# Optimization experiments

Hardware: AMD Instinct MI355X
Metric: run time of the kernel (lower is better)

## Reference

```python
import jax, jax.numpy as jnp
import numpy as np

B = 32          # batch of input networks (INRs)
D = 128         # d_hid
H = 8           # attention heads
DH = D // H
L = 3           # RT layers
DOUT = 10
LAYOUT = [2, 32, 32, 1]          # INR layer layout -> graph nodes
N = 2 + 32 + 32 + 1              # 67 nodes
POS_LAYOUT = [1, 1, 32, 32, 1]   # [1]*layout[0] + layout[1:-1] + [1]*layout[-1]


def _ln(x, g, b, eps=1e-5):
    m = x.mean(-1, keepdims=True)
    v = ((x - m) ** 2).mean(-1, keepdims=True)
    return (x - m) * jax.lax.rsqrt(v + eps) * g + b


def _gelu(x):
    return jax.nn.gelu(x, approximate=False)


def setup_inputs() -> dict:
    key = jax.random.key(0)
    cnt = [0]
    def nk():
        cnt[0] += 1
        return jax.random.fold_in(key, cnt[0])
    def rn(shape, s=0.02):
        return (s * jax.random.normal(nk(), shape)).astype(jnp.float32)
    z = lambda *s: jnp.zeros(s, jnp.float32)
    o = lambda *s: jnp.ones(s, jnp.float32)
    inp = dict(
        w0=rn((B, 2, 32, 1), 1.0), w1=rn((B, 32, 32, 1), 1.0), w2=rn((B, 32, 1, 1), 1.0),
        b0=rn((B, 32, 1), 1.0), b1=rn((B, 32, 1), 1.0), b2=rn((B, 1, 1), 1.0),
        pw_W=rn((1, D)), pw_b=z(D), pb_W=rn((1, D)), pb_b=z(D),
        node_in_W=rn((D, D)), node_in_b=z(D), edge_in_W=rn((D, D)), edge_in_b=z(D),
        pos_embed=rn((len(POS_LAYOUT), D), 1.0),
        aln_g=o(L, D), aln_b=z(L, D),
        Wqkv_n=rn((L, D, 3 * D)), Wqkv_e=rn((L, D, 3 * D)), Wao=rn((L, D, D)), bao=z(L, D),
        Wl0=rn((L, D, D)), bl0=z(L, D),
        nln_g=o(L, D), nln_b=z(L, D),
        nW1=rn((L, D, 2 * D)), nb1=z(L, 2 * D), nW2=rn((L, 2 * D, D)), nb2=z(L, D),
        eln_g=o(L, D), eln_b=z(L, D),
        We=rn((L, 2 * D, D)), be=z(L, D),
        Ws=rn((L, D, D)), bs=z(L, D), Wt=rn((L, D, D)), bt=z(L, D),
        Wer=rn((L, D, D)), Wec=rn((L, D, D)), We1=rn((L, D, D)), be1=z(L, D),
        Wel0=rn((L, D, D)), bel0=z(L, D),
        mln_g=o(L, D), mln_b=z(L, D),
        mW1=rn((L, D, 2 * D)), mb1=z(L, 2 * D), mW2=rn((L, 2 * D, D)), mb2=z(L, D),
        Wo1=rn((D, D)), bo1=z(D), Wo2=rn((D, DOUT)), bo2=z(DOUT),
    )
    return inp


def _forward(w0, w1, w2, b0, b1, b2, pw_W, pw_b, pb_W, pb_b, node_in_W, node_in_b,
             edge_in_W, edge_in_b, pos_embed, aln_g, aln_b, Wqkv_n, Wqkv_e, Wao, bao,
             Wl0, bl0, nln_g, nln_b, nW1, nb1, nW2, nb2, eln_g, eln_b, We, be, Ws, bs,
             Wt, bt, Wer, Wec, We1, be1, Wel0, bel0, mln_g, mln_b, mW1, mb1, mW2, mb2,
             Wo1, bo1, Wo2, bo2):
    # ---- GraphConstructor / batch_to_graphs (layout [2,32,32,1], offsets 0/2/34/66) ----
    nf = jnp.zeros((B, N, 1), w0.dtype)
    ef = jnp.zeros((B, N, N, 1), w0.dtype)
    ef = ef.at[:, 0:2, 2:34].set(w0).at[:, 2:34, 34:66].set(w1).at[:, 34:66, 66:67].set(w2)
    nf = nf.at[:, 2:34].set(b0).at[:, 34:66].set(b1).at[:, 66:67].set(b2)
    node = nf @ pb_W + pb_b            # proj_bias: Linear(1, D)
    edge = ef @ pw_W + pw_b            # proj_weight: Linear(1, D)
    node = node @ node_in_W + node_in_b
    edge = edge @ edge_in_W + edge_in_b
    pos = jnp.concatenate([jnp.broadcast_to(pos_embed[i], (n, D))
                           for i, n in enumerate(POS_LAYOUT)], axis=0)  # [N, D]
    node = node + pos

    scale = 1.0 / np.sqrt(DH)
    for l in range(L):
        # ---- RTAttention (edge-biased multi-head attention) ----
        h = _ln(node, aln_g[l], aln_b[l])
        qkv_n = (h @ Wqkv_n[l]).reshape(B, N, H, 3, DH).transpose(0, 2, 3, 1, 4)       # b H 3 n dh
        qn, kn, vn = qkv_n[:, :, 0], qkv_n[:, :, 1], qkv_n[:, :, 2]
        qkv_e = (edge @ Wqkv_e[l]).reshape(B, N, N, H, 3, DH).transpose(0, 3, 4, 1, 2, 5)  # b H 3 n m dh
        q = qn[:, :, :, None, :] + qkv_e[:, :, 0]
        k = kn[:, :, None, :, :] + qkv_e[:, :, 1]
        v = vn[:, :, None, :, :] + qkv_e[:, :, 2]
        att = jax.nn.softmax((q * k).sum(-1) * scale, axis=-1)                          # b H n m
        o = jnp.einsum('bhnm,bhnmd->bhnd', att, v).transpose(0, 2, 1, 3).reshape(B, N, D)
        node = node + ((o @ Wao[l] + bao[l]) @ Wl0[l] + bl0[l])
        node = node + (_gelu(_ln(node, nln_g[l], nln_b[l]) @ nW1[l] + nb1[l]) @ nW2[l] + nb2[l])
        # ---- Edge update (EdgeMLP with forward/reversed edges + node/row/col terms) ----
        en = _ln(edge, eln_g[l], eln_b[l])
        m = jnp.concatenate([en, en.transpose(0, 2, 1, 3)], axis=-1) @ We[l] + be[l]
        m = m + (node @ Ws[l] + bs[l])[:, :, None, :] + (node @ Wt[l] + bt[l])[:, None, :, :]
        m = m + en.mean(2, keepdims=True) @ Wer[l] + en.mean(1, keepdims=True) @ Wec[l]
        m = _gelu(m) @ We1[l] + be1[l]
        edge = edge + (m @ Wel0[l] + bel0[l])
        edge = edge + (_gelu(_ln(edge, mln_g[l], mln_b[l]) @ mW1[l] + mb1[l]) @ mW2[l] + mb2[l])

    g = node.mean(1)                                        # mean pooling over nodes
    return jax.nn.relu(g @ Wo1 + bo1) @ Wo2 + bo2           # [B, DOUT]


def reference(w0, w1, w2, b0, b1, b2, pw_W, pw_b, pb_W, pb_b, node_in_W, node_in_b,
              edge_in_W, edge_in_b, pos_embed, aln_g, aln_b, Wqkv_n, Wqkv_e, Wao, bao,
              Wl0, bl0, nln_g, nln_b, nW1, nb1, nW2, nb2, eln_g, eln_b, We, be, Ws, bs,
              Wt, bt, Wer, Wec, We1, be1, Wel0, bel0, mln_g, mln_b, mW1, mb1, mW2, mb2,
              Wo1, bo1, Wo2, bo2):
    return _forward(w0, w1, w2, b0, b1, b2, pw_W, pw_b, pb_W, pb_b, node_in_W, node_in_b,
                    edge_in_W, edge_in_b, pos_embed, aln_g, aln_b, Wqkv_n, Wqkv_e, Wao, bao,
                    Wl0, bl0, nln_g, nln_b, nW1, nb1, nW2, nb2, eln_g, eln_b, We, be, Ws, bs,
                    Wt, bt, Wer, Wec, We1, be1, Wel0, bel0, mln_g, mln_b, mW1, mb1, mW2, mb2,
                    Wo1, bo1, Wo2, bo2)
```

## Files before the change

### kernel.cpp

```cpp
#include <hip/hip_runtime.h>
#include <math.h>

constexpr int B_ = 32, N_ = 67, D_ = 128, H_ = 8, DH_ = 16, L_ = 3;
constexpr int NN_ = N_ * N_;
constexpr int RN_ = B_ * N_;
constexpr int RE_ = B_ * NN_;
constexpr int DOUT_ = 10;

typedef __attribute__((ext_vector_type(8))) short short8;
typedef __attribute__((ext_vector_type(4))) float f32x4;

__device__ __forceinline__ float gelu_f(float x) {
  float u = x * (0.7978845608028654f + 0.035677408136f * x * x);
  float e = __expf(-2.f * u);
  return x * (1.f / (1.f + e));
}
__device__ __forceinline__ ushort f2b(float x) {
  union { float f; unsigned u; } v; v.f = x;
  return (ushort)((v.u + 0x7FFFu + ((v.u >> 16) & 1u)) >> 16);
}
__device__ __forceinline__ float b2f(ushort u) {
  union { unsigned u; float f; } v; v.u = (unsigned)u << 16; return v.f;
}

__global__ void k_comb(const float* __restrict__ Wao, const float* __restrict__ bao,
                       const float* __restrict__ Wl0, const float* __restrict__ bl0,
                       const float* __restrict__ We1, const float* __restrict__ be1,
                       const float* __restrict__ Wel0, const float* __restrict__ bel0,
                       float* WcN, float* bcN, float* WcE, float* bcE) {
  int t = blockIdx.x * blockDim.x + threadIdx.x;
  const int half = L_ * D_ * D_;
  if (t >= 2 * half) return;
  int which = t / half;
  int u = t - which * half;
  int l = u / (D_ * D_);
  int ij = u - l * (D_ * D_);
  int i = ij >> 7, j = ij & 127;
  const float* A  = (which == 0 ? Wao : We1) + (size_t)l * D_ * D_;
  const float* Bm = (which == 0 ? Wl0 : Wel0) + (size_t)l * D_ * D_;
  float s = 0.f;
  for (int k = 0; k < D_; k++) s += A[i * D_ + k] * Bm[k * D_ + j];
  if (which == 0) WcN[u] = s; else WcE[u] = s;
  if (i == 0) {
    const float* ba = (which == 0 ? bao : be1) + l * D_;
    const float* bl = (which == 0 ? bl0 : bel0) + l * D_;
    float sb = 0.f;
    for (int k = 0; k < D_; k++) sb += ba[k] * Bm[k * D_ + j];
    if (which == 0) bcN[l * D_ + j] = sb + bl[j]; else bcE[l * D_ + j] = sb + bl[j];
  }
}

__device__ __forceinline__ float enc_src(const float* src, int K, int C, int NKS, int r, int l) {
  int frag = r >> 9;
  int within = r & 511;
  int lane = within >> 3, j = within & 7;
  int cf = frag / NKS, ks = frag - cf * NKS;
  int k = ks * 32 + (lane >> 4) * 8 + j;
  int c = cf * 16 + (lane & 15);
  return src[(size_t)l * K * C + (size_t)k * C + c];
}

__global__ void k_prepw(const float* __restrict__ Wqkve, const float* __restrict__ We,
                        const float* __restrict__ WcE, const float* __restrict__ mW1,
                        const float* __restrict__ mW2,
                        ushort* wq, ushort* we, ushort* wce, ushort* w1, ushort* w2) {
  int t = blockIdx.x * 256 + threadIdx.x;
  const int S0 = L_ * 49152, S1 = L_ * 32768, S2 = L_ * 16384, S3 = L_ * 32768, S4 = L_ * 32768;
  if (t < S0) { int l = t / 49152, r = t % 49152; wq[t]  = f2b(enc_src(Wqkve, 128, 384, 4, r, l)); return; }
  t -= S0;
  if (t < S1) { int l = t / 32768, r = t % 32768; we[t]  = f2b(enc_src(We,   256, 128, 8, r, l)); return; }
  t -= S1;
  if (t < S2) { int l = t / 16384, r = t % 16384; wce[t] = f2b(enc_src(WcE,  128, 128, 4, r, l)); return; }
  t -= S2;
  if (t < S3) { int l = t / 32768, r = t % 32768; w1[t]  = f2b(enc_src(mW1,  128, 256, 4, r, l)); return; }
  t -= S3;
  if (t < S4) { int l = t / 32768, r = t % 32768; w2[t]  = f2b(enc_src(mW2,  256, 128, 8, r, l)); return; }
}

__global__ void k_vecs(const float* pbW, const float* pbb, const float* niW, const float* nib,
                       const float* pwW, const float* pwb, const float* eiW, const float* eib,
                       float* vecs) {
  int j = threadIdx.x;
  if (j >= D_) return;
  float u = 0, c = 0, v = 0, ce = 0;
  for (int k = 0; k < D_; k++) {
    u  += pbW[k] * niW[k * D_ + j];
    c  += pbb[k] * niW[k * D_ + j];
    v  += pwW[k] * eiW[k * D_ + j];
    ce += pwb[k] * eiW[k * D_ + j];
  }
  vecs[j] = u; vecs[D_ + j] = c + nib[j]; vecs[2 * D_ + j] = v; vecs[3 * D_ + j] = ce + eib[j];
}

__global__ void k_init_node(const float* __restrict__ b0, const float* __restrict__ b1,
                            const float* __restrict__ b2, const float* __restrict__ vecs,
                            const float* __restrict__ pos, float* __restrict__ node) {
  int idx = blockIdx.x * blockDim.x + threadIdx.x;
  if (idx >= RN_ * D_) return;
  int r = idx >> 7, d = idx & 127;
  int b = r / N_, n = r - b * N_;
  float nf = 0.f;
  if (n >= 2 && n < 34)       nf = b0[b * 32 + n - 2];
  else if (n >= 34 && n < 66) nf = b1[b * 32 + n - 34];
  else if (n == 66)           nf = b2[b];
  int pr = (n == 0) ? 0 : (n == 1) ? 1 : (n < 34) ? 2 : (n < 66) ? 3 : 4;
  node[idx] = nf * vecs[d] + vecs[D_ + d] + pos[pr * D_ + d];
}

__global__ void k_init_edge(const float* __restrict__ w0, const float* __restrict__ w1,
                            const float* __restrict__ w2, const float* __restrict__ vecs,
                            ushort* __restrict__ edge) {
  int idx = blockIdx.x * blockDim.x + threadIdx.x;
  if (idx >= RE_ * D_) return;
  int r = idx >> 7, d = idx & 127;
  int b = r / NN_;
  int rem = r - b * NN_;
  int n = rem / N_, m = rem - n * N_;
  float ef = 0.f;
  if (n < 2)        { if (m >= 2 && m < 34)  ef = w0[(b * 2 + n) * 32 + (m - 2)]; }
  else if (n < 34)  { if (m >= 34 && m < 66) ef = w1[(b * 32 + (n - 2)) * 32 + (m - 34)]; }
  else if (n < 66)  { if (m == 66)           ef = w2[b * 32 + (n - 34)]; }
  edge[idx] = f2b(ef * vecs[2 * D_ + d] + vecs[3 * D_ + d]);
}

__global__ __launch_bounds__(256) void k_lnqkv(
    const float* __restrict__ node, const float* __restrict__ g, const float* __restrict__ bb,
    const float* __restrict__ W, float* __restrict__ out) {
  __shared__ float As[16][68];
  __shared__ float Wsh[16][68];
  __shared__ float stmu[64], strs[64];
  int r0 = blockIdx.x * 64, c0 = blockIdx.y * 64;
  int tid = threadIdx.x;
  {
    int row = tid >> 2, part = tid & 3;
    int gr = r0 + row;
    int grc = (gr < RN_) ? gr : 0;
    const float* x = node + (size_t)grc * 128 + part * 32;
    float s = 0.f, q = 0.f;
#pragma unroll
    for (int i = 0; i < 8; i++) {
      float4 v = *reinterpret_cast<const float4*>(&x[i * 4]);
      s += v.x + v.y + v.z + v.w;
      q += v.x * v.x + v.y * v.y + v.z * v.z + v.w * v.w;
    }
    for (int o = 1; o < 4; o <<= 1) { s += __shfl_xor(s, o); q += __shfl_xor(q, o); }
    if (part == 0) {
      float mu = s * (1.f / 128.f);
      stmu[row] = mu;
      strs[row] = rsqrtf(q * (1.f / 128.f) - mu * mu + 1e-5f);
    }
  }
  __syncthreads();
  int tr = tid >> 4, tc = tid & 15;
  float acc[4][4] = {};
  for (int kk = 0; kk < 128; kk += 16) {
#pragma unroll
    for (int i = 0; i < 4; i++) {
      int lin = tid + i * 256;
      int r_in = lin >> 4, k_in = lin & 15;
      int r = r0 + r_in;
      float v = 0.f;
      if (r < RN_) {
        int k = kk + k_in;
        v = (node[(size_t)r * 128 + k] - stmu[r_in]) * strs[r_in] * g[k] + bb[k];
      }
      As[k_in][r_in] = v;
    }
#pragma unroll
    for (int i = 0; i < 4; i++) {
      int lin = tid + i * 256;
      int k_in = lin >> 6, c_in = lin & 63;
      Wsh[k_in][c_in] = W[(size_t)(kk + k_in) * 384 + c0 + c_in];
    }
    __syncthreads();
#pragma unroll
    for (int k = 0; k < 16; k++) {
      float4 a4 = *reinterpret_cast<const float4*>(&As[k][tr * 4]);
      float4 b4 = *reinterpret_cast<const float4*>(&Wsh[k][tc * 4]);
      float av[4] = {a4.x, a4.y, a4.z, a4.w};
      float bv[4] = {b4.x, b4.y, b4.z, b4.w};
#pragma unroll
      for (int i = 0; i < 4; i++)
#pragma unroll
        for (int j = 0; j < 4; j++) acc[i][j] += av[i] * bv[j];
    }
    __syncthreads();
  }
#pragma unroll
  for (int i = 0; i < 4; i++) {
    int r = r0 + tr * 4 + i;
    if (r >= RN_) continue;
#pragma unroll
    for (int j = 0; j < 4; j++) {
      int c = c0 + tc * 4 + j;
      out[(size_t)r * 384 + c] = acc[i][j];
    }
  }
}

__global__ __launch_bounds__(256) void k_nodemlp(
    float* __restrict__ node, const float* __restrict__ obuf,
    const float* __restrict__ WcN, const float* __restrict__ bcN,
    const float* __restrict__ g, const float* __restrict__ bb,
    const float* __restrict__ nW1, const float* __restrict__ nb1,
    const float* __restrict__ nW2, const float* __restrict__ nb2) {
  __shared__ float As[16][17];
  __shared__ float Wsh[16][132];
  __shared__ ushort Hs[16][136];
  __shared__ ushort Ts[16][264];
  int r0 = blockIdx.x * 16;
  int tid = threadIdx.x;
  int tr = tid >> 4, tc = tid & 15;
  size_t grow = (size_t)(r0 + tr) * 128;

  auto stageW = [&](const float* src, int ld, int kk, int cbase) {
    int k = tid & 15, cp = tid >> 4;
    const float* s = &src[(size_t)(kk + k) * ld + cbase + cp * 8];
    float* d = &Wsh[k][cp * 8];
#pragma unroll
    for (int j = 0; j < 8; j++) d[j] = s[j];
  };

  float acc[8] = {};
  for (int kk = 0; kk < 128; kk += 16) {
    As[tr][tc] = obuf[grow + kk + tc];
    stageW(WcN, 128, kk, 0);
    __syncthreads();
#pragma unroll
    for (int k = 0; k < 16; k++) {
      float a = As[tr][k];
#pragma unroll
      for (int j = 0; j < 8; j++) acc[j] += a * Wsh[k][tc * 8 + j];
    }
    __syncthreads();
  }
  float nd[8];
  float s = 0.f, q = 0.f;
#pragma unroll
  for (int j = 0; j < 8; j++) {
    int c = tc * 8 + j;
    float v = node[grow + c] + acc[j] + bcN[c];
    nd[j] = v; s += v; q += v * v;
  }
  for (int o = 1; o < 16; o <<= 1) { s += __shfl_xor(s, o); q += __shfl_xor(q, o); }
  float mu = s * (1.f / 128.f);
  float rs = rsqrtf(q * (1.f / 128.f) - mu * mu + 1e-5f);
#pragma unroll
  for (int j = 0; j < 8; j++) {
    int c = tc * 8 + j;
    Hs[tr][c] = f2b((nd[j] - mu) * rs * g[c] + bb[c]);
  }
  for (int ch = 0; ch < 2; ch++) {
    float a2[8] = {};
    for (int kk = 0; kk < 128; kk += 16) {
      __syncthreads();
      stageW(nW1, 256, kk, ch * 128);
      __syncthreads();
#pragma unroll
      for (int k = 0; k < 16; k++) {
        float a = b2f(Hs[tr][kk + k]);
#pragma unroll
        for (int j = 0; j < 8; j++) a2[j] += a * Wsh[k][tc * 8 + j];
      }
    }
#pragma unroll
    for (int j = 0; j < 8; j++) {
      int c = ch * 128 + tc * 8 + j;
      Ts[tr][c] = f2b(gelu_f(a2[j] + nb1[c]));
    }
  }
  float a3[8] = {};
  for (int kk = 0; kk < 256; kk += 16) {
    __syncthreads();
    stageW(nW2, 128, kk, 0);
    __syncthreads();
#pragma unroll
    for (int k = 0; k < 16; k++) {
      float a = b2f(Ts[tr][kk + k]);
#pragma unroll
      for (int j = 0; j < 8; j++) a3[j] += a * Wsh[k][tc * 8 + j];
    }
  }
#pragma unroll
  for (int j = 0; j < 8; j++) {
    int c = tc * 8 + j;
    node[grow + c] = nd[j] + a3[j] + nb2[c];
  }
}

__global__ __launch_bounds__(256) void k_nvec(
    const float* __restrict__ node, const float* __restrict__ rmean, const float* __restrict__ cmean,
    const float* __restrict__ Ws, const float* __restrict__ Wer,
    const float* __restrict__ Wt, const float* __restrict__ Wec,
    const float* __restrict__ bs, const float* __restrict__ be, const float* __restrict__ bt,
    float* __restrict__ rvec, float* __restrict__ cvec) {
  __shared__ float Ash[16][68];
  __shared__ float Wsh[16][68];
  int which = blockIdx.z;
  const float* A2 = which ? cmean : rmean;
  const float* W1 = which ? Wt : Ws;
  const float* W2 = which ? Wec : Wer;
  float* out = which ? cvec : rvec;
  int r0 = blockIdx.x * 64, c0 = blockIdx.y * 64;
  int tid = threadIdx.x, tr = tid >> 4, tc = tid & 15;
  float acc[4][4] = {};
  for (int kk = 0; kk < 256; kk += 16) {
#pragma unroll
    for (int i = 0; i < 4; i++) {
      int lin = tid + i * 256;
      int r_in = lin >> 4, k_in = lin & 15;
      int r = r0 + r_in, k = kk + k_in;
      float v = 0.f;
      if (r < RN_) v = (k < 128) ? node[(size_t)r * 128 + k] : A2[(size_t)r * 128 + (k - 128)];
      Ash[k_in][r_in] = v;
    }
#pragma unroll
    for (int i = 0; i < 4; i++) {
      int lin = tid + i * 256;
      int k_in = lin >> 6, c_in = lin & 63;
      int k = kk + k_in, c = c0 + c_in;
      Wsh[k_in][c_in] = (k < 128) ? W1[(size_t)k * 128 + c] : W2[(size_t)(k - 128) * 128 + c];
    }
    __syncthreads();
#pragma unroll
    for (int k = 0; k < 16; k++) {
      float4 a4 = *reinterpret_cast<const float4*>(&Ash[k][tr * 4]);
      float4 b4 = *reinterpret_cast<const float4*>(&Wsh[k][tc * 4]);
      float av[4] = {a4.x, a4.y, a4.z, a4.w};
      float bv[4] = {b4.x, b4.y, b4.z, b4.w};
#pragma unroll
      for (int i = 0; i < 4; i++)
#pragma unroll
        for (int j = 0; j < 4; j++) acc[i][j] += av[i] * bv[j];
    }
    __syncthreads();
  }
#pragma unroll
  for (int i = 0; i < 4; i++) {
    int r = r0 + tr * 4 + i;
    if (r >= RN_) continue;
#pragma unroll
    for (int j = 0; j < 4; j++) {
      int c = c0 + tc * 4 + j;
      float bias = which ? bt[c] : (bs[c] + be[c]);
      out[(size_t)r * 128 + c] = acc[i][j] + bias;
    }
  }
}

__global__ __launch_bounds__(256, 3) void k_eattn(
    const ushort* __restrict__ edge, const float* __restrict__ qkvn,
    const ushort* __restrict__ wqf,
    const float* __restrict__ gE, const float* __restrict__ bE,
    float* __restrict__ stats, float* __restrict__ rmean,
    float* __restrict__ obuf) {
  __shared__ __align__(16) ushort ed[68 * 128];
  __shared__ __align__(16) ushort Eb[68 * 202];
  __shared__ float qn_s[384];
  __shared__ float sc[4][68];
  __shared__ float red[4][16][4];
  __shared__ float stmu[68], strs[68];
  int bn = blockIdx.x;
  int b = bn / N_;
  int tid = threadIdx.x;
  int w = tid >> 6, lane = tid & 63, lr = lane & 15, lk8 = (lane >> 4) * 8;
  int swz = (lr & 7) << 3;
  int rb = (lane >> 4) * 4;
  size_t ebase = (size_t)bn * N_ * 128;

  for (int i = 0; i < 5; i++) {
    int u = tid + i * 256;
    if (u < 67 * 16) {
      int row = u >> 4, k8 = (u & 15) * 8;
      short8 t = __builtin_nontemporal_load(
          reinterpret_cast<const short8*>(&edge[ebase + (size_t)row * 128 + k8]));
      *reinterpret_cast<short8*>(&ed[row * 128 + (k8 ^ ((row & 7) << 3))]) = t;
      float s = 0.f, q = 0.f;
#pragma unroll
      for (int j = 0; j < 8; j++) { float v = b2f((ushort)t[j]); s += v; q += v * v; }
      for (int o = 8; o; o >>= 1) { s += __shfl_xor(s, o); q += __shfl_xor(q, o); }
      if ((u & 15) == 0) {
        float mu = s * (1.f / 128.f);
        float rs = rsqrtf(q * (1.f / 128.f) - mu * mu + 1e-5f);
        stmu[row] = mu; strs[row] = rs;
        stats[2 * (size_t)(bn * N_ + row)] = mu;
        stats[2 * (size_t)(bn * N_ + row) + 1] = rs;
      }
    }
  }
  for (int i = tid; i < 384; i += 256) qn_s[i] = qkvn[(size_t)bn * 384 + i];
  __syncthreads();
  if (tid < 128) {
    float s = 0.f;
    for (int m = 0; m < 67; m++)
      s += (b2f(ed[m * 128 + (tid ^ ((m & 7) << 3))]) - stmu[m]) * strs[m];
    rmean[(size_t)bn * 128 + tid] = gE[tid] * (s * (1.f / 67.f)) + bE[tid];
  }

  for (int ch = 0; ch < 2; ch++) {
    int h0 = ch * 4;
    f32x4 acc[5][3] = {};
    __builtin_amdgcn_s_setprio(1);
#pragma unroll
    for (int ks = 0; ks < 4; ks++) {
      int kof = ks * 32 + lk8;
      short8 af[5];
#pragma unroll
      for (int rf = 0; rf < 5; rf++)
        af[rf] = *reinterpret_cast<const short8*>(&ed[(rf * 16 + lr) * 128 + (kof ^ swz)]);
#pragma unroll
      for (int cl = 0; cl < 3; cl++) {
        short8 bf = *reinterpret_cast<const short8*>(
            &wqf[(size_t)(((ch * 12 + w * 3 + cl) * 4 + ks) * 64 + lane) * 8]);
#pragma unroll
        for (int rf = 0; rf < 5; rf++)
          acc[rf][cl] = __builtin_amdgcn_mfma_f32_16x16x32_bf16(af[rf], bf, acc[rf][cl], 0, 0, 0);
      }
    }
    __builtin_amdgcn_s_setprio(0);
#pragma unroll
    for (int rf = 0; rf < 5; rf++)
#pragma unroll
      for (int cl = 0; cl < 3; cl++) {
        int colc = (w * 3 + cl) * 16 + lr;
#pragma unroll
        for (int rg = 0; rg < 4; rg++) {
          int er = rf * 16 + rb + rg;
          if (er < 67) Eb[er * 202 + colc] = f2b(acc[rf][cl][rg]);
        }
      }
    __syncthreads();
    for (int idx = tid; idx < 268; idx += 256) {
      int h2 = idx / 67, m = idx - h2 * 67;
      const ushort* e = &Eb[m * 202 + h2 * 48];
      const float* kn = &qkvn[(size_t)(b * N_ + m) * 384 + (h0 + h2) * 48 + 16];
      const float* qn = &qn_s[(h0 + h2) * 48];
      float s2 = 0.f;
#pragma unroll
      for (int d = 0; d < 16; d++)
        s2 += (qn[d] + b2f(e[d])) * (kn[d] + b2f(e[16 + d]));
      sc[h2][m] = s2 * 0.25f;
    }
    __syncthreads();
    {
      float v0 = (lane < 67) ? sc[w][lane] : -1e30f;
      float v1 = (lane < 3) ? sc[w][lane + 64] : -1e30f;
      float mx = fmaxf(v0, v1);
      for (int o = 32; o; o >>= 1) mx = fmaxf(mx, __shfl_xor(mx, o));
      float e0 = (lane < 67) ? __expf(v0 - mx) : 0.f;
      float e1 = (lane < 3) ? __expf(v1 - mx) : 0.f;
      float ss = e0 + e1;
      for (int o = 32; o; o >>= 1) ss += __shfl_xor(ss, o);
      float inv = 1.f / ss;
      if (lane < 67) sc[w][lane] = e0 * inv;
      if (lane < 3) sc[w][lane + 64] = e1 * inv;
    }
    __syncthreads();
    {
      int item = tid >> 2, c = tid & 3;
      int h2 = item >> 4, d = item & 15;
      float p = 0.f;
      for (int m = c; m < 67; m += 4) {
        float v = qkvn[(size_t)(b * N_ + m) * 384 + (h0 + h2) * 48 + 32 + d]
                + b2f(Eb[m * 202 + h2 * 48 + 32 + d]);
        p += sc[h2][m] * v;
      }
      red[h2][d][c] = p;
    }
    __syncthreads();
    if (tid < 64) {
      int h2 = tid >> 4, d = tid & 15;
      obuf[(size_t)bn * 128 + (h0 + h2) * 16 + d] =
          red[h2][d][0] + red[h2][d][1] + red[h2][d][2] + red[h2][d][3];
    }
    __syncthreads();
  }
}

__global__ void k_colmean(const ushort* __restrict__ edge, const float* __restrict__ stats,
                          const float* __restrict__ g, const float* __restrict__ bb,
                          float* __restrict__ cmean) {
  int bm = blockIdx.x;
  int b = bm / N_, m = bm - b * N_;
  int d = threadIdx.x;
  float s = 0.f;
  for (int n = 0; n < N_; n++) {
    size_t r = (size_t)b * NN_ + (size_t)n * N_ + m;
    s += (b2f(edge[r * D_ + d]) - stats[2 * r]) * stats[2 * r + 1];
  }
  cmean[(size_t)bm * D_ + d] = g[d] * (s * (1.f / 67.f)) + bb[d];
}

__global__ __launch_bounds__(256, 2) void k_fedge(
    const ushort* __restrict__ ein, ushort* __restrict__ eout,
    const float* __restrict__ stats,
    const float* __restrict__ gE, const float* __restrict__ bE,
    const ushort* __restrict__ wef,
    const float* __restrict__ rvec, const float* __restrict__ cvec,
    const ushort* __restrict__ wcef,
    const float* __restrict__ bcE,
    const float* __restrict__ gM, const float* __restrict__ bM,
    const ushort* __restrict__ w1f,
    const float* __restrict__ mb1,
    const ushort* __restrict__ w2f,
    const float* __restrict__ mb2) {
  __shared__ __align__(16) ushort As[64 * 256];
  __shared__ __align__(16) ushort mt[64 * 128];
  __shared__ __align__(16) ushort Wb[32 * 512];
  int tid = threadIdx.x;
  int r0 = blockIdx.x * 64;
  int w = tid >> 6, lane = tid & 63, lr = lane & 15, lk8 = (lane >> 4) * 8;
  int swz = (lr & 7) << 3;
  int rb = (lane >> 4) * 4;
  int arow = w * 16 + lr;

  auto stageW = [&](const ushort* src) {
#pragma unroll
    for (int i = 0; i < 8; i++) {
      int u = tid + i * 256;
      short8 t = *reinterpret_cast<const short8*>(&src[(size_t)u * 8]);
      *reinterpret_cast<short8*>(&Wb[u * 8]) = t;
    }
  };

#pragma unroll
  for (int i = 0; i < 8; i++) {
    int u = tid + i * 256;
    int row = u >> 5, c8 = (u & 31) * 8;
    int gr = r0 + row;
    int grc = (gr < RE_) ? gr : 0;
    int cc = c8 & 127;
    short8 t;
    float mu, rs;
    if (c8 < 128) {
      size_t srow = (size_t)grc;
      mu = stats[2 * srow]; rs = stats[2 * srow + 1];
      t = *reinterpret_cast<const short8*>(&ein[srow * 128 + cc]);
    } else {
      int b = grc / NN_; int rem = grc - b * NN_;
      int n = rem / N_, m = rem - n * N_;
      size_t srow = (size_t)b * NN_ + (size_t)m * N_ + n;
      mu = stats[2 * srow]; rs = stats[2 * srow + 1];
      t = __builtin_nontemporal_load(reinterpret_cast<const short8*>(&ein[srow * 128 + cc]));
    }
    short8 r8;
#pragma unroll
    for (int j = 0; j < 8; j++) {
      float v = (b2f((ushort)t[j]) - mu) * rs * gE[cc + j] + bE[cc + j];
      r8[j] = (short)f2b(v);
    }
    *reinterpret_cast<short8*>(&As[row * 256 + (c8 ^ ((row & 7) << 3))]) = r8;
  }
  int rvb[4], cvb[4], grows[4]; bool vr[4];
#pragma unroll
  for (int rg = 0; rg < 4; rg++) {
    int gr = r0 + w * 16 + rb + rg;
    vr[rg] = gr < RE_;
    int grc = vr[rg] ? gr : 0;
    grows[rg] = grc;
    int b = grc / NN_; int rem = grc - b * NN_;
    int n = rem / N_, m = rem - n * N_;
    rvb[rg] = (b * N_ + n) * 128;
    cvb[rg] = (b * N_ + m) * 128;
  }
  __syncthreads();

  for (int h = 0; h < 2; h++) {
    if (h) __syncthreads();
    stageW(wef + (size_t)h * 32 * 512);
    __syncthreads();
    f32x4 acc[4] = {};
    __builtin_amdgcn_s_setprio(1);
#pragma unroll
    for (int ks = 0; ks < 8; ks++) {
      int kof = ks * 32 + lk8;
      short8 af = *reinterpret_cast<const short8*>(&As[arow * 256 + (kof ^ swz)]);
#pragma unroll
      for (int cf = 0; cf < 4; cf++) {
        short8 bf = *reinterpret_cast<const short8*>(&Wb[(cf * 8 + ks) * 512 + lane * 8]);
        acc[cf] = __builtin_amdgcn_mfma_f32_16x16x32_bf16(af, bf, acc[cf], 0, 0, 0);
      }
    }
    __builtin_amdgcn_s_setprio(0);
#pragma unroll
    for (int cf = 0; cf < 4; cf++) {
      int c = (h * 4 + cf) * 16 + lr;
#pragma unroll
      for (int rg = 0; rg < 4; rg++) {
        float v = acc[cf][rg] + rvec[rvb[rg] + c] + cvec[cvb[rg] + c];
        int mrow = w * 16 + rb + rg;
        mt[mrow * 128 + (c ^ ((mrow & 7) << 3))] = f2b(gelu_f(v));
      }
    }
  }

  __syncthreads();
  stageW(wcef);
  __syncthreads();
  f32x4 e1[8] = {};
  __builtin_amdgcn_s_setprio(1);
#pragma unroll
  for (int ks = 0; ks < 4; ks++) {
    int kof = ks * 32 + lk8;
    short8 af = *reinterpret_cast<const short8*>(&mt[arow * 128 + (kof ^ swz)]);
#pragma unroll
    for (int cf = 0; cf < 8; cf++) {
      short8 bf = *reinterpret_cast<const short8*>(&Wb[(cf * 4 + ks) * 512 + lane * 8]);
      e1[cf] = __builtin_amdgcn_mfma_f32_16x16x32_bf16(af, bf, e1[cf], 0, 0, 0);
    }
  }
  __builtin_amdgcn_s_setprio(0);
  {
    float sr[4] = {0, 0, 0, 0}, qr[4] = {0, 0, 0, 0};
#pragma unroll
    for (int cf = 0; cf < 8; cf++) {
      int c = cf * 16 + lr;
#pragma unroll
      for (int rg = 0; rg < 4; rg++) {
        float v = e1[cf][rg] + bcE[c] + b2f(ein[(size_t)grows[rg] * 128 + c]);
        e1[cf][rg] = v;
        sr[rg] += v; qr[rg] += v * v;
      }
    }
#pragma unroll
    for (int rg = 0; rg < 4; rg++) {
      float s = sr[rg], q = qr[rg];
      for (int o = 8; o; o >>= 1) { s += __shfl_xor(s, o); q += __shfl_xor(q, o); }
      float mu = s * (1.f / 128.f);
      float rs = rsqrtf(q * (1.f / 128.f) - mu * mu + 1e-5f);
#pragma unroll
      for (int cf = 0; cf < 8; cf++) {
        int c = cf * 16 + lr;
        int mrow = w * 16 + rb + rg;
        mt[mrow * 128 + (c ^ ((mrow & 7) << 3))] =
            f2b((e1[cf][rg] - mu) * rs * gM[c] + bM[c]);
      }
    }
  }

  for (int h = 0; h < 2; h++) {
    __syncthreads();
    stageW(w1f + (size_t)h * 32 * 512);
    __syncthreads();
    f32x4 acc[8] = {};
    __builtin_amdgcn_s_setprio(1);
#pragma unroll
    for (int ks = 0; ks < 4; ks++) {
      int kof = ks * 32 + lk8;
      short8 af = *reinterpret_cast<const short8*>(&mt[arow * 128 + (kof ^ swz)]);
#pragma unroll
      for (int cf = 0; cf < 8; cf++) {
        short8 bf = *reinterpret_cast<const short8*>(&Wb[(cf * 4 + ks) * 512 + lane * 8]);
        acc[cf] = __builtin_amdgcn_mfma_f32_16x16x32_bf16(af, bf, acc[cf], 0, 0, 0);
      }
    }
    __builtin_amdgcn_s_setprio(0);
#pragma unroll
    for (int cf = 0; cf < 8; cf++) {
      int c2 = (h * 8 + cf) * 16 + lr;
#pragma unroll
      for (int rg = 0; rg < 4; rg++) {
        int mrow = w * 16 + rb + rg;
        As[mrow * 256 + (c2 ^ ((mrow & 7) << 3))] = f2b(gelu_f(acc[cf][rg] + mb1[c2]));
      }
    }
  }

  for (int h = 0; h < 2; h++) {
    __syncthreads();
    stageW(w2f + (size_t)h * 32 * 512);
    __syncthreads();
    f32x4 acc[4] = {};
    __builtin_amdgcn_s_setprio(1);
#pragma unroll
    for (int ks = 0; ks < 8; ks++) {
      int kof = ks * 32 + lk8;
      short8 af = *reinterpret_cast<const short8*>(&As[arow * 256 + (kof ^ swz)]);
#pragma unroll
      for (int cf = 0; cf < 4; cf++) {
        short8 bf = *reinterpret_cast<const short8*>(&Wb[(cf * 8 + ks) * 512 + lane * 8]);
        acc[cf] = __builtin_amdgcn_mfma_f32_16x16x32_bf16(af, bf, acc[cf], 0, 0, 0);
      }
    }
    __builtin_amdgcn_s_setprio(0);
#pragma unroll
    for (int cf = 0; cf < 4; cf++) {
      int cg = h * 4 + cf;
      int c = cg * 16 + lr;
#pragma unroll
      for (int rg = 0; rg < 4; rg++) {
        int mrow = w * 16 + rb + rg;
        mt[mrow * 128 + (c ^ ((mrow & 7) << 3))] = f2b(e1[cg][rg] + acc[cf][rg] + mb2[c]);
      }
    }
  }

  __syncthreads();
#pragma unroll
  for (int p = 0; p < 4; p++) {
    int u = p * 256 + tid;
    int row = u >> 4, col8 = (u & 15) * 8;
    int gr = r0 + row;
    if (gr < RE_) {
      short8 v = *reinterpret_cast<const short8*>(&mt[row * 128 + (col8 ^ ((row & 7) << 3))]);
      __builtin_nontemporal_store(v, reinterpret_cast<short8*>(&eout[(size_t)gr * 128 + col8]));
    }
  }
}

__global__ void k_head(const float* __restrict__ node, const float* __restrict__ Wo1,
                       const float* __restrict__ bo1, const float* __restrict__ Wo2,
                       const float* __restrict__ bo2, float* __restrict__ out) {
  int b = blockIdx.x;
  int tid = threadIdx.x;
  __shared__ float gsh[D_];
  __shared__ float h1[D_];
  float s = 0.f;
  for (int n = 0; n < N_; n++) s += node[((size_t)b * N_ + n) * D_ + tid];
  gsh[tid] = s * (1.f / 67.f);
  __syncthreads();
  float a = 0.f;
  for (int k = 0; k < D_; k++) a += gsh[k] * Wo1[k * D_ + tid];
  h1[tid] = fmaxf(a + bo1[tid], 0.f);
  __syncthreads();
  if (tid < DOUT_) {
    float r = 0.f;
    for (int k = 0; k < D_; k++) r += h1[k] * Wo2[k * DOUT_ + tid];
    out[b * DOUT_ + tid] = r + bo2[tid];
  }
}

extern "C" void kernel_launch(void* const* d_in, const int* in_sizes, int n_in,
                              void* d_out, int out_size, void* d_ws, size_t ws_size,
                              hipStream_t stream) {
  const float* w0   = (const float*)d_in[0];
  const float* w1   = (const float*)d_in[1];
  const float* w2   = (const float*)d_in[2];
  const float* b0   = (const float*)d_in[3];
  const float* b1   = (const float*)d_in[4];
  const float* b2   = (const float*)d_in[5];
  const float* pwW  = (const float*)d_in[6];
  const float* pwb  = (const float*)d_in[7];
  const float* pbW  = (const float*)d_in[8];
  const float* pbb  = (const float*)d_in[9];
  const float* niW  = (const float*)d_in[10];
  const float* nib  = (const float*)d_in[11];
  const float* eiW  = (const float*)d_in[12];
  const float* eib  = (const float*)d_in[13];
  const float* pos  = (const float*)d_in[14];
  const float* alng = (const float*)d_in[15];
  const float* alnb = (const float*)d_in[16];
  const float* Wqkvn= (const float*)d_in[17];
  const float* Wqkve= (const float*)d_in[18];
  const float* Wao  = (const float*)d_in[19];
  const float* bao  = (const float*)d_in[20];
  const float* Wl0  = (const float*)d_in[21];
  const float* bl0  = (const float*)d_in[22];
  const float* nlng = (const float*)d_in[23];
  const float* nlnb = (const float*)d_in[24];
  const float* nW1  = (const float*)d_in[25];
  const float* nb1  = (const float*)d_in[26];
  const float* nW2  = (const float*)d_in[27];
  const float* nb2  = (const float*)d_in[28];
  const float* elng = (const float*)d_in[29];
  const float* elnb = (const float*)d_in[30];
  const float* We   = (const float*)d_in[31];
  const float* be   = (const float*)d_in[32];
  const float* Ws   = (const float*)d_in[33];
  const float* bs   = (const float*)d_in[34];
  const float* Wt   = (const float*)d_in[35];
  const float* bt   = (const float*)d_in[36];
  const float* Wer  = (const float*)d_in[37];
  const float* Wec  = (const float*)d_in[38];
  const float* We1  = (const float*)d_in[39];
  const float* be1  = (const float*)d_in[40];
  const float* Wel0 = (const float*)d_in[41];
  const float* bel0 = (const float*)d_in[42];
  const float* mlng = (const float*)d_in[43];
  const float* mlnb = (const float*)d_in[44];
  const float* mW1  = (const float*)d_in[45];
  const float* mb1  = (const float*)d_in[46];
  const float* mW2  = (const float*)d_in[47];
  const float* mb2  = (const float*)d_in[48];
  const float* Wo1  = (const float*)d_in[49];
  const float* bo1  = (const float*)d_in[50];
  const float* Wo2  = (const float*)d_in[51];
  const float* bo2  = (const float*)d_in[52];
  float* outp = (float*)d_out;

  const size_t E = (size_t)RE_ * D_;
  const size_t NODE = (size_t)RN_ * D_;
  const int DD = D_ * D_;

  float* ws = (float*)d_ws;
  size_t off = 0;
  auto alloc = [&](size_t nf) { float* p = ws + off; off += nf; return p; };
  ushort* edgeA = (ushort*)alloc(E / 2);
  ushort* edgeB = (ushort*)alloc(E / 2);
  float* stats = alloc(2 * (size_t)RE_);
  float* node  = alloc(NODE);
  float* qkvn  = alloc(3 * NODE);
  float* obuf  = alloc(NODE);
  float* rmean = alloc(NODE);
  float* cmean = alloc(NODE);
  float* rvec  = alloc(NODE);
  float* cvec  = alloc(NODE);
  float* WcN   = alloc((size_t)L_ * DD);
  float* bcN   = alloc((size_t)L_ * D_);
  float* WcE   = alloc((size_t)L_ * DD);
  float* bcE   = alloc((size_t)L_ * D_);
  float* vecs  = alloc(4 * D_);
  ushort* wbf   = (ushort*)alloc(245760);
  ushort* wq_fm = wbf;
  ushort* we_fm = wq_fm + (size_t)L_ * 49152;
  ushort* wce_fm= we_fm + (size_t)L_ * 32768;
  ushort* w1_fm = wce_fm + (size_t)L_ * 16384;
  ushort* w2_fm = w1_fm + (size_t)L_ * 32768;
  (void)ws_size; (void)in_sizes; (void)n_in; (void)out_size;

  k_comb<<<(2 * L_ * DD + 255) / 256, 256, 0, stream>>>(Wao, bao, Wl0, bl0, We1, be1, Wel0, bel0,
                                                        WcN, bcN, WcE, bcE);
  k_prepw<<<1920, 256, 0, stream>>>(Wqkve, We, WcE, mW1, mW2, wq_fm, we_fm, wce_fm, w1_fm, w2_fm);
  k_vecs<<<1, 128, 0, stream>>>(pbW, pbb, niW, nib, pwW, pwb, eiW, eib, vecs);
  k_init_node<<<(RN_ * D_ + 255) / 256, 256, 0, stream>>>(b0, b1, b2, vecs, pos, node);
  k_init_edge<<<(int)((E + 255) / 256), 256, 0, stream>>>(w0, w1, w2, vecs, edgeA);

  const int GE = (RE_ + 63) / 64;
  const int GN = (RN_ + 63) / 64;
  const int GM = RN_ / 16;

  for (int l = 0; l < L_; l++) {
    ushort* ein  = (l & 1) ? edgeB : edgeA;
    ushort* eout = (l & 1) ? edgeA : edgeB;
    const float* Wqn = Wqkvn + (size_t)l * D_ * 384;

    k_lnqkv<<<dim3(GN, 6), 256, 0, stream>>>(node, alng + l * D_, alnb + l * D_, Wqn, qkvn);
    k_eattn<<<RN_, 256, 0, stream>>>(ein, qkvn, wq_fm + (size_t)l * 49152,
                                     elng + l * D_, elnb + l * D_, stats, rmean, obuf);
    k_nodemlp<<<GM, 256, 0, stream>>>(node, obuf, WcN + (size_t)l * DD, bcN + l * D_,
                                      nlng + l * D_, nlnb + l * D_,
                                      nW1 + (size_t)l * D_ * 256, nb1 + l * 256,
                                      nW2 + (size_t)l * 256 * D_, nb2 + l * D_);

    k_colmean<<<RN_, 128, 0, stream>>>(ein, stats, elng + l * D_, elnb + l * D_, cmean);
    k_nvec<<<dim3(GN, 2, 2), 256, 0, stream>>>(node, rmean, cmean,
                                               Ws + (size_t)l * DD, Wer + (size_t)l * DD,
                                               Wt + (size_t)l * DD, Wec + (size_t)l * DD,
                                               bs + l * D_, be + l * D_, bt + l * D_,
                                               rvec, cvec);

    k_fedge<<<GE, 256, 0, stream>>>(ein, eout, stats,
                                    elng + l * D_, elnb + l * D_,
                                    we_fm + (size_t)l * 32768, rvec, cvec,
                                    wce_fm + (size_t)l * 16384, bcE + l * D_,
                                    mlng + l * D_, mlnb + l * D_,
                                    w1_fm + (size_t)l * 32768, mb1 + l * 256,
                                    w2_fm + (size_t)l * 32768, mb2 + l * D_);
  }

  k_head<<<B_, 128, 0, stream>>>(node, Wo1, bo1, Wo2, bo2, outp);
}
```

Before: 1.003 ms.

## Keep edge-attention scores, softmax and PV in registers per wave-head

The edge-attention kernel now assigns one head per wave and computes the q·k score, softmax, and value aggregation straight from the MFMA accumulators using cross-lane shuffles. This removes the Eb/sc/red shared-memory staging and several block-wide barriers. The smaller shared-memory footprint allows raising the launch bound to four blocks per CU. In exchange the K and V node rows are read from global memory per lane with scattered loads, and register pressure rises under the tighter occupancy bound.

```diff
diff --git a/kernel.cpp b/kernel.cpp
--- a/kernel.cpp
+++ b/kernel.cpp
@@ -348,17 +348,13 @@
   }
 }
 
-__global__ __launch_bounds__(256, 3) void k_eattn(
+__global__ __launch_bounds__(256, 4) void k_eattn(
     const ushort* __restrict__ edge, const float* __restrict__ qkvn,
     const ushort* __restrict__ wqf,
     const float* __restrict__ gE, const float* __restrict__ bE,
     float* __restrict__ stats, float* __restrict__ rmean,
     float* __restrict__ obuf) {
   __shared__ __align__(16) ushort ed[68 * 128];
-  __shared__ __align__(16) ushort Eb[68 * 202];
-  __shared__ float qn_s[384];
-  __shared__ float sc[4][68];
-  __shared__ float red[4][16][4];
   __shared__ float stmu[68], strs[68];
   int bn = blockIdx.x;
   int b = bn / N_;
@@ -388,7 +384,6 @@
       }
     }
   }
-  for (int i = tid; i < 384; i += 256) qn_s[i] = qkvn[(size_t)bn * 384 + i];
   __syncthreads();
   if (tid < 128) {
     float s = 0.f;
@@ -397,8 +392,8 @@
     rmean[(size_t)bn * 128 + tid] = gE[tid] * (s * (1.f / 67.f)) + bE[tid];
   }
 
-  for (int ch = 0; ch < 2; ch++) {
-    int h0 = ch * 4;
+  for (int hh = 0; hh < 2; hh++) {
+    int h = w + hh * 4;
     f32x4 acc[5][3] = {};
     __builtin_amdgcn_s_setprio(1);
 #pragma unroll
@@ -411,69 +406,58 @@
 #pragma unroll
       for (int cl = 0; cl < 3; cl++) {
         short8 bf = *reinterpret_cast<const short8*>(
-            &wqf[(size_t)(((ch * 12 + w * 3 + cl) * 4 + ks) * 64 + lane) * 8]);
+            &wqf[(size_t)(((h * 3 + cl) * 4 + ks) * 64 + lane) * 8]);
 #pragma unroll
         for (int rf = 0; rf < 5; rf++)
           acc[rf][cl] = __builtin_amdgcn_mfma_f32_16x16x32_bf16(af[rf], bf, acc[rf][cl], 0, 0, 0);
       }
     }
     __builtin_amdgcn_s_setprio(0);
+    float qn_d = qkvn[(size_t)bn * 384 + h * 48 + lr];
+    float att[5][4];
+    float mx = -1e30f;
+#pragma unroll
+    for (int rf = 0; rf < 5; rf++) {
+#pragma unroll
+      for (int rg = 0; rg < 4; rg++) {
+        int m = rf * 16 + rb + rg;
+        float kn = (m < 67) ? qkvn[(size_t)(b * N_ + m) * 384 + h * 48 + 16 + lr] : 0.f;
+        float p = (qn_d + acc[rf][0][rg]) * (kn + acc[rf][1][rg]);
+        for (int o = 8; o; o >>= 1) p += __shfl_xor(p, o);
+        p = (m < 67) ? p * 0.25f : -1e30f;
+        att[rf][rg] = p;
+        mx = fmaxf(mx, p);
+      }
+    }
+    mx = fmaxf(mx, __shfl_xor(mx, 16));
+    mx = fmaxf(mx, __shfl_xor(mx, 32));
+    float ssum = 0.f;
 #pragma unroll
     for (int rf = 0; rf < 5; rf++)
 #pragma unroll
-      for (int cl = 0; cl < 3; cl++) {
-        int colc = (w * 3 + cl) * 16 + lr;
-#pragma unroll
-        for (int rg = 0; rg < 4; rg++) {
-          int er = rf * 16 + rb + rg;
-          if (er < 67) Eb[er * 202 + colc] = f2b(acc[rf][cl][rg]);
+      for (int rg = 0; rg < 4; rg++) {
+        int m = rf * 16 + rb + rg;
+        float e = (m < 67) ? __expf(att[rf][rg] - mx) : 0.f;
+        att[rf][rg] = e;
+        ssum += e;
+      }
+    ssum += __shfl_xor(ssum, 16);
+    ssum += __shfl_xor(ssum, 32);
+    float inv = 1.f / ssum;
+    float oacc = 0.f;
+#pragma unroll
+    for (int rf = 0; rf < 5; rf++)
+#pragma unroll
+      for (int rg = 0; rg < 4; rg++) {
+        int m = rf * 16 + rb + rg;
+        if (m < 67) {
+          float vn = qkvn[(size_t)(b * N_ + m) * 384 + h * 48 + 32 + lr];
+          oacc += att[rf][rg] * (vn + acc[rf][2][rg]);
         }
       }
-    __syncthreads();
-    for (int idx = tid; idx < 268; idx += 256) {
-      int h2 = idx / 67, m = idx - h2 * 67;
-      const ushort* e = &Eb[m * 202 + h2 * 48];
-      const float* kn = &qkvn[(size_t)(b * N_ + m) * 384 + (h0 + h2) * 48 + 16];
-      const float* qn = &qn_s[(h0 + h2) * 48];
-      float s2 = 0.f;
-#pragma unroll
-      for (int d = 0; d < 16; d++)
-        s2 += (qn[d] + b2f(e[d])) * (kn[d] + b2f(e[16 + d]));
-      sc[h2][m] = s2 * 0.25f;
-    }
-    __syncthreads();
-    {
-      float v0 = (lane < 67) ? sc[w][lane] : -1e30f;
-      float v1 = (lane < 3) ? sc[w][lane + 64] : -1e30f;
-      float mx = fmaxf(v0, v1);
-      for (int o = 32; o; o >>= 1) mx = fmaxf(mx, __shfl_xor(mx, o));
-      float e0 = (lane < 67) ? __expf(v0 - mx) : 0.f;
-      float e1 = (lane < 3) ? __expf(v1 - mx) : 0.f;
-      float ss = e0 + e1;
-      for (int o = 32; o; o >>= 1) ss += __shfl_xor(ss, o);
-      float inv = 1.f / ss;
-      if (lane < 67) sc[w][lane] = e0 * inv;
-      if (lane < 3) sc[w][lane + 64] = e1 * inv;
-    }
-    __syncthreads();
-    {
-      int item = tid >> 2, c = tid & 3;
-      int h2 = item >> 4, d = item & 15;
-      float p = 0.f;
-      for (int m = c; m < 67; m += 4) {
-        float v = qkvn[(size_t)(b * N_ + m) * 384 + (h0 + h2) * 48 + 32 + d]
-                + b2f(Eb[m * 202 + h2 * 48 + 32 + d]);
-        p += sc[h2][m] * v;
-      }
-      red[h2][d][c] = p;
-    }
-    __syncthreads();
-    if (tid < 64) {
-      int h2 = tid >> 4, d = tid & 15;
-      obuf[(size_t)bn * 128 + (h0 + h2) * 16 + d] =
-          red[h2][d][0] + red[h2][d][1] + red[h2][d][2] + red[h2][d][3];
-    }
-    __syncthreads();
+    oacc += __shfl_xor(oacc, 16);
+    oacc += __shfl_xor(oacc, 32);
+    if (lane < 16) obuf[(size_t)bn * 128 + h * 16 + lr] = oacc * inv;
   }
 }
 
```

Measured after the change: 1.304 ms. 1.3x slower.
